# Kernel tuning notes

Hardware: AMD Instinct MI355X
Metric: run time of the kernel (lower is better)

## Reference

```python
import jax, jax.numpy as jnp
import numpy as np

B, S, D = 2, 2048, 1024
H = 16
DH = D // H  # 64


def setup_inputs() -> dict:
    key = jax.random.key(0)
    ks = jax.random.split(key, 5)
    scale = 0.02
    x = jax.random.normal(ks[0], (B, S, D), dtype=jnp.float32)
    W_qkv = jax.random.normal(ks[1], (D, 3 * D), dtype=jnp.float32) * scale
    b_qkv = jnp.zeros((3 * D,), dtype=jnp.float32)
    W_out = jax.random.normal(ks[2], (D, D), dtype=jnp.float32) * scale
    b_out = jnp.zeros((D,), dtype=jnp.float32)
    return {"x": x, "W_qkv": W_qkv, "b_qkv": b_qkv, "W_out": W_out, "b_out": b_out}


def reference(x, W_qkv, b_qkv, W_out, b_out):
    # Fused QKV projection: [B,S,D] @ [D,3D] -> [B,S,3D]
    qkv = jnp.einsum('bsd,df->bsf', x, W_qkv) + b_qkv
    q, k, v = qkv[:, :, :D], qkv[:, :, D:2 * D], qkv[:, :, 2 * D:]
    # Split heads: [B,S,D] -> [B,H,S,DH]
    def split(t):
        return t.reshape(B, S, H, DH).transpose(0, 2, 1, 3)
    q, k, v = split(q), split(k), split(v)
    # Scaled dot-product attention (naive, full score matrix as in source)
    scores = jnp.einsum('bhqd,bhkd->bhqk', q, k) / jnp.sqrt(jnp.float32(DH))
    probs = jax.nn.softmax(scores, axis=-1)  # mask=None, dropout eval-mode identity
    attn = jnp.einsum('bhqk,bhkd->bhqd', probs, v)
    # Merge heads: [B,H,S,DH] -> [B,S,D]
    attn = attn.transpose(0, 2, 1, 3).reshape(B, S, D)
    out = jnp.einsum('bsd,de->bse', attn, W_out) + b_out
    return out
```

## Files before the change

### kernel.cpp

```cpp
#include <hip/hip_runtime.h>

typedef _Float16 half8  __attribute__((ext_vector_type(8)));
typedef _Float16 half4  __attribute__((ext_vector_type(4)));
typedef float    floatx4  __attribute__((ext_vector_type(4)));
typedef float    floatx16 __attribute__((ext_vector_type(16)));
typedef unsigned int uint4v __attribute__((ext_vector_type(4)));

constexpr int B_ = 2, S_ = 2048, D_ = 1024, H_ = 16, M_ = 4096;
constexpr int NR_ = B_ * H_ * S_;
constexpr float QSCALE = 0.18033688011112042f;
constexpr int KVB = 64;
constexpr int HT = 16;

__device__ __forceinline__ void gload16(const void* g, void* l) {
  __builtin_amdgcn_global_load_lds((const __attribute__((address_space(1))) void*)g,
                                   (__attribute__((address_space(3))) void*)l, 16, 0, 0);
}

__global__ __launch_bounds__(256) void cast_f32_f16(const float* __restrict__ in,
                                                    _Float16* __restrict__ out, int n8) {
  int i = blockIdx.x * 256 + threadIdx.x;
  if (i >= n8) return;
  float4 a = reinterpret_cast<const float4*>(in)[2 * i];
  float4 b = reinterpret_cast<const float4*>(in)[2 * i + 1];
  half8 h;
  h[0] = (_Float16)a.x; h[1] = (_Float16)a.y; h[2] = (_Float16)a.z; h[3] = (_Float16)a.w;
  h[4] = (_Float16)b.x; h[5] = (_Float16)b.y; h[6] = (_Float16)b.z; h[7] = (_Float16)b.w;
  reinterpret_cast<half8*>(out)[i] = h;
}

__global__ __launch_bounds__(256) void transpose_cast2(const float* __restrict__ W0,
                                                       _Float16* __restrict__ WT0,
                                                       const float* __restrict__ W1,
                                                       _Float16* __restrict__ WT1) {
  __shared__ float Ws[64][65];
  const int z = blockIdx.z;
  const int NW = z ? D_ : 3 * D_;
  if (blockIdx.x * 64 >= NW) return;
  const float* W = z ? W1 : W0;
  _Float16* WT = z ? WT1 : WT0;
  const int K = D_, N = NW;
  const int n0 = blockIdx.x * 64, k0 = blockIdx.y * 64;
  const int t = threadIdx.x;
#pragma unroll
  for (int i = 0; i < 4; i++) {
    int idx = t + 256 * i;
    int r = idx >> 4, c4 = idx & 15;
    float4 v = *reinterpret_cast<const float4*>(W + (size_t)(k0 + r) * N + n0 + c4 * 4);
    Ws[r][c4 * 4 + 0] = v.x; Ws[r][c4 * 4 + 1] = v.y;
    Ws[r][c4 * 4 + 2] = v.z; Ws[r][c4 * 4 + 3] = v.w;
  }
  __syncthreads();
#pragma unroll
  for (int i = 0; i < 2; i++) {
    int idx = t + 256 * i;
    int r = idx >> 3, ck = idx & 7;
    half8 h;
#pragma unroll
    for (int j = 0; j < 8; j++) h[j] = (_Float16)Ws[ck * 8 + j][r];
    *reinterpret_cast<half8*>(WT + (size_t)(n0 + r) * K + k0 + ck * 8) = h;
  }
}

__global__ __launch_bounds__(512, 2) void gemm256_mfma(
    const _Float16* __restrict__ A, const _Float16* __restrict__ BT,
    const float* __restrict__ bias, _Float16* __restrict__ Cout,
    int M, int N, int K, float scale_lo, int ncut) {
  extern __shared__ char smem[];
  const int tid = threadIdx.x, w = tid >> 6, lane = tid & 63;
  const int wm = w >> 2, wn = w & 3;

  const int nwg = gridDim.x, cpx = nwg >> 3;
  const int wg = (blockIdx.x & 7) * cpx + (blockIdx.x >> 3);
  const int nbx = N / 192;
  const int bx = wg % nbx, by = wg / nbx;
  const int m0 = by * 256, n0 = bx * 192;

  const int NT = K >> 6;

  auto stageA1 = [&](int buf, int kt, int i) {
    const int k0 = kt * 64;
    char* Ad = smem + buf * 32768;
    int idx = tid + 512 * i;
    int r = idx >> 3, c = idx & 7, cs = c ^ (r & 7);
    gload16(A + (size_t)(m0 + r) * K + k0 + cs * 8, Ad + idx * 16);
  };
  auto stageB1 = [&](int buf, int kt, int i) {
    const int k0 = kt * 64;
    char* Bd = smem + 65536 + buf * 24576;
    int idx = tid + 512 * i;
    int r = idx >> 3, c = idx & 7, cs = c ^ (r & 7);
    gload16(BT + (size_t)(n0 + r) * K + k0 + cs * 8, Bd + idx * 16);
  };

  floatx4 acc[8][3] = {};

#pragma unroll
  for (int i = 0; i < 4; i++) stageA1(0, 0, i);
#pragma unroll
  for (int i = 0; i < 3; i++) stageB1(0, 0, i);

  for (int kt = 0; kt < NT; ++kt) {
    const int p = kt & 1;
    asm volatile("s_waitcnt vmcnt(0)" ::: "memory");
    __builtin_amdgcn_s_barrier();
    __builtin_amdgcn_sched_barrier(0);

    const char* Ab = smem + p * 32768;
    const char* Bb = smem + 65536 + p * 24576;
    const bool more = (kt + 1 < NT);
#pragma unroll
    for (int q = 0; q < 4; q++) {
      half8 af[2][2], bf[3][2];
#pragma unroll
      for (int e = 0; e < 2; e++)
#pragma unroll
        for (int ks = 0; ks < 2; ks++) {
          int row = wm * 128 + (2 * q + e) * 16 + (lane & 15);
          int ch = (ks * 4 + (lane >> 4)) ^ (row & 7);
          af[e][ks] = *reinterpret_cast<const half8*>(Ab + row * 128 + ch * 16);
        }
#pragma unroll
      for (int n = 0; n < 3; n++)
#pragma unroll
        for (int ks = 0; ks < 2; ks++) {
          int row = wn * 48 + n * 16 + (lane & 15);
          int ch = (ks * 4 + (lane >> 4)) ^ (row & 7);
          bf[n][ks] = *reinterpret_cast<const half8*>(Bb + row * 128 + ch * 16);
        }
      if (more) {
        if (q == 0)      { stageA1(p ^ 1, kt + 1, 0); stageA1(p ^ 1, kt + 1, 1); }
        else if (q == 1) { stageA1(p ^ 1, kt + 1, 2); stageA1(p ^ 1, kt + 1, 3); }
        else if (q == 2) { stageB1(p ^ 1, kt + 1, 0); stageB1(p ^ 1, kt + 1, 1); }
        else             { stageB1(p ^ 1, kt + 1, 2); }
      }
      __builtin_amdgcn_s_setprio(1);
#pragma unroll
      for (int ks = 0; ks < 2; ks++)
#pragma unroll
        for (int e = 0; e < 2; e++)
#pragma unroll
          for (int n = 0; n < 3; n++)
            acc[2 * q + e][n] = __builtin_amdgcn_mfma_f32_16x16x32_f16(
                af[e][ks], bf[n][ks], acc[2 * q + e][n], 0, 0, 0);
      __builtin_amdgcn_s_setprio(0);
    }
    __builtin_amdgcn_sched_barrier(0);
    __builtin_amdgcn_s_barrier();
  }

#pragma unroll
  for (int mf = 0; mf < 8; mf++)
#pragma unroll
    for (int n = 0; n < 3; n++) {
      int col = n0 + wn * 48 + n * 16 + (lane & 15);
      float bv = bias[col];
      float sc = (col < ncut) ? scale_lo : 1.0f;
#pragma unroll
      for (int reg = 0; reg < 4; reg++) {
        int row = m0 + wm * 128 + mf * 16 + (lane >> 4) * 4 + reg;
        Cout[(size_t)row * N + col] = (_Float16)((acc[mf][n][reg] + bv) * sc);
      }
    }
}

template <bool OUT_HALF>
__global__ __launch_bounds__(256) void gemm_mfma(const _Float16* __restrict__ A,
                                                 const _Float16* __restrict__ BT,
                                                 const float* __restrict__ bias,
                                                 void* __restrict__ Cout,
                                                 int M, int N, int K,
                                                 float scale_lo, int ncut) {
  __shared__ _Float16 As[128 * 64];
  __shared__ _Float16 Bs[128 * 64];
  const int t = threadIdx.x, w = t >> 6, lane = t & 63;
  const int m0 = blockIdx.y * 128, n0 = blockIdx.x * 128;
  const int wr = (w >> 1) * 64, wc = (w & 1) * 64;

  floatx4 acc[4][4] = {};

  for (int k0 = 0; k0 < K; k0 += 64) {
    __syncthreads();
#pragma unroll
    for (int i = 0; i < 4; i++) {
      int idx = t + 256 * i;
      int r = idx >> 3, c = idx & 7;
      int cs = c ^ (r & 7);
      gload16(A + (size_t)(m0 + r) * K + k0 + cs * 8, (char*)As + idx * 16);
      gload16(BT + (size_t)(n0 + r) * K + k0 + cs * 8, (char*)Bs + idx * 16);
    }
    __syncthreads();
#pragma unroll
    for (int ks = 0; ks < 2; ks++) {
      half8 af[4], bf[4];
#pragma unroll
      for (int r = 0; r < 4; r++) {
        int row = wr + r * 16 + (lane & 15);
        int ch = (ks * 4 + (lane >> 4)) ^ (row & 7);
        af[r] = *reinterpret_cast<const half8*>((const char*)As + row * 128 + ch * 16);
      }
#pragma unroll
      for (int c = 0; c < 4; c++) {
        int row = wc + c * 16 + (lane & 15);
        int ch = (ks * 4 + (lane >> 4)) ^ (row & 7);
        bf[c] = *reinterpret_cast<const half8*>((const char*)Bs + row * 128 + ch * 16);
      }
#pragma unroll
      for (int r = 0; r < 4; r++)
#pragma unroll
        for (int c = 0; c < 4; c++)
          acc[r][c] = __builtin_amdgcn_mfma_f32_16x16x32_f16(af[r], bf[c], acc[r][c], 0, 0, 0);
    }
  }

#pragma unroll
  for (int r = 0; r < 4; r++)
#pragma unroll
    for (int c = 0; c < 4; c++) {
      int col = n0 + wc + c * 16 + (lane & 15);
      float bv = bias[col];
      float sc = (col < ncut) ? scale_lo : 1.0f;
#pragma unroll
      for (int reg = 0; reg < 4; reg++) {
        int row = m0 + wr + r * 16 + (lane >> 4) * 4 + reg;
        float v = (acc[r][c][reg] + bv) * sc;
        if (OUT_HALF)
          reinterpret_cast<_Float16*>(Cout)[(size_t)row * N + col] = (_Float16)v;
        else
          reinterpret_cast<float*>(Cout)[(size_t)row * N + col] = v;
      }
    }
}

__global__ __launch_bounds__(256) void v_transpose(const _Float16* __restrict__ qkv,
                                                   _Float16* __restrict__ Vt) {
  __shared__ _Float16 Vs[64][72];
  const int s0 = blockIdx.x * 64, bh = blockIdx.y;
  const int b = bh >> 4, h = bh & 15;
  const int t = threadIdx.x;
#pragma unroll
  for (int i = 0; i < 2; i++) {
    int idx = t + 256 * i;
    int r = idx >> 3, c = idx & 7;
    half8 v = *reinterpret_cast<const half8*>(
        qkv + (size_t)(b * S_ + s0 + r) * (3 * D_) + 2 * D_ + h * 64 + c * 8);
    *reinterpret_cast<half8*>(&Vs[r][c * 8]) = v;
  }
  __syncthreads();
#pragma unroll
  for (int i = 0; i < 2; i++) {
    int idx = t + 256 * i;
    int d = idx >> 3, c = idx & 7;
    half8 o;
#pragma unroll
    for (int j = 0; j < 8; j++) o[j] = Vs[c * 8 + j][d];
    *reinterpret_cast<half8*>(Vt + ((size_t)bh * 64 + d) * S_ + s0 + c * 8) = o;
  }
}

__global__ __launch_bounds__(256, 4) void flash_mfma(const _Float16* __restrict__ qkv,
                                                     const _Float16* __restrict__ Vt,
                                                     _Float16* __restrict__ Opart,
                                                     float* __restrict__ keys) {
  const int qt = blockIdx.x, h = blockIdx.y;
  const int b = blockIdx.z >> 1, sp = blockIdx.z & 1;
  const int t = threadIdx.x, w = t >> 6, lane = t & 63;
  const int lo = lane & 31, hi = lane >> 5;

  __shared__ _Float16 Ks[2][KVB * 64];
  __shared__ _Float16 Vts[2][64 * KVB];

  const int qrow = qt * 128 + w * 32 + lo;
  const _Float16* qbase = qkv + (size_t)(b * S_ + qrow) * (3 * D_) + h * 64;
  half8 qf[4];
#pragma unroll
  for (int kd = 0; kd < 4; kd++)
    qf[kd] = *reinterpret_cast<const half8*>(qbase + kd * 16 + hi * 8);
  asm volatile("" : "+v"(qf[0]), "+v"(qf[1]), "+v"(qf[2]), "+v"(qf[3]));

  const size_t kbase = (size_t)(b * S_) * (3 * D_) + D_ + h * 64;
  const size_t vbase = (size_t)(b * H_ + h) * 64 * S_;
  const int kvbase = sp * (S_ / 2);

  auto stage = [&](int buf, int tile) {
    const int kv0 = kvbase + tile * KVB;
    const _Float16* kg = qkv + kbase + (size_t)kv0 * (3 * D_);
#pragma unroll
    for (int p = 0; p < 2; p++) {
      int idx = t + 256 * p;
      int r = idx >> 3, c = idx & 7, cs = c ^ (r & 7);
      gload16(kg + (size_t)r * (3 * D_) + cs * 8, (char*)&Ks[buf][0] + idx * 16);
    }
    const _Float16* vg = Vt + vbase + kv0;
#pragma unroll
    for (int p = 0; p < 2; p++) {
      int idx = t + 256 * p;
      int r = idx >> 3, c = idx & 7, cs = c ^ (r & 7);
      gload16(vg + (size_t)r * S_ + cs * 8, (char*)&Vts[buf][0] + idx * 16);
    }
  };

  floatx16 o0, o1;
#pragma unroll
  for (int r = 0; r < 16; r++) { o0[r] = 0.f; o1[r] = 0.f; }
  float m = -1e30f, l = 0.f;

  stage(0, 0);

  for (int tt = 0; tt < HT; ++tt) {
    const int cb = tt & 1;
    stage(cb ^ 1, (tt + 1) & (HT - 1));
    asm volatile("s_waitcnt vmcnt(4)" ::: "memory");
    __builtin_amdgcn_s_barrier();
    __builtin_amdgcn_sched_barrier(0);

    const char* kb2 = (const char*)&Ks[cb][0];
    floatx16 s0v, s1v;
#pragma unroll
    for (int r = 0; r < 16; r++) { s0v[r] = 0.f; s1v[r] = 0.f; }
    __builtin_amdgcn_s_setprio(1);
#pragma unroll
    for (int kd = 0; kd < 4; kd++) {
      int r0 = lo, r1 = 32 + lo;
      half8 k0f = *reinterpret_cast<const half8*>(
          kb2 + r0 * 128 + (((kd * 2 + hi) ^ (r0 & 7)) * 16));
      half8 k1f = *reinterpret_cast<const half8*>(
          kb2 + r1 * 128 + (((kd * 2 + hi) ^ (r1 & 7)) * 16));
      s0v = __builtin_amdgcn_mfma_f32_32x32x16_f16(k0f, qf[kd], s0v, 0, 0, 0);
      s1v = __builtin_amdgcn_mfma_f32_32x32x16_f16(k1f, qf[kd], s1v, 0, 0, 0);
    }
    __builtin_amdgcn_s_setprio(0);

    float pm = -1e30f;
#pragma unroll
    for (int r = 0; r < 16; r++) pm = fmaxf(pm, fmaxf(s0v[r], s1v[r]));
    pm = fmaxf(pm, __shfl_xor(pm, 32));
    if (!__all(pm <= m + 8.0f)) {
      float mn = fmaxf(m, pm);
      float al = __builtin_amdgcn_exp2f(m - mn);
      m = mn; l *= al;
#pragma unroll
      for (int r = 0; r < 16; r++) { o0[r] *= al; o1[r] *= al; }
    }
    float rs = 0.f;
#pragma unroll
    for (int r = 0; r < 16; r++) {
      s0v[r] = __builtin_amdgcn_exp2f(s0v[r] - m);
      s1v[r] = __builtin_amdgcn_exp2f(s1v[r] - m);
      rs += s0v[r] + s1v[r];
    }
    rs += __shfl_xor(rs, 32);
    l += rs;

    half8 pf0a, pf0b, pf1a, pf1b;
    {
      unsigned a0 = __builtin_bit_cast(unsigned, __builtin_amdgcn_cvt_pkrtz(s0v[0], s0v[1]));
      unsigned b0 = __builtin_bit_cast(unsigned, __builtin_amdgcn_cvt_pkrtz(s0v[4], s0v[5]));
      unsigned a1 = __builtin_bit_cast(unsigned, __builtin_amdgcn_cvt_pkrtz(s0v[2], s0v[3]));
      unsigned b1 = __builtin_bit_cast(unsigned, __builtin_amdgcn_cvt_pkrtz(s0v[6], s0v[7]));
      asm("v_permlane32_swap_b32 %0, %1" : "+v"(a0), "+v"(b0));
      asm("v_permlane32_swap_b32 %0, %1" : "+v"(a1), "+v"(b1));
      uint4v u; u[0] = a0; u[1] = a1; u[2] = b0; u[3] = b1;
      pf0a = __builtin_bit_cast(half8, u);
      a0 = __builtin_bit_cast(unsigned, __builtin_amdgcn_cvt_pkrtz(s0v[8], s0v[9]));
      b0 = __builtin_bit_cast(unsigned, __builtin_amdgcn_cvt_pkrtz(s0v[12], s0v[13]));
      a1 = __builtin_bit_cast(unsigned, __builtin_amdgcn_cvt_pkrtz(s0v[10], s0v[11]));
      b1 = __builtin_bit_cast(unsigned, __builtin_amdgcn_cvt_pkrtz(s0v[14], s0v[15]));
      asm("v_permlane32_swap_b32 %0, %1" : "+v"(a0), "+v"(b0));
      asm("v_permlane32_swap_b32 %0, %1" : "+v"(a1), "+v"(b1));
      u[0] = a0; u[1] = a1; u[2] = b0; u[3] = b1;
      pf0b = __builtin_bit_cast(half8, u);
      a0 = __builtin_bit_cast(unsigned, __builtin_amdgcn_cvt_pkrtz(s1v[0], s1v[1]));
      b0 = __builtin_bit_cast(unsigned, __builtin_amdgcn_cvt_pkrtz(s1v[4], s1v[5]));
      a1 = __builtin_bit_cast(unsigned, __builtin_amdgcn_cvt_pkrtz(s1v[2], s1v[3]));
      b1 = __builtin_bit_cast(unsigned, __builtin_amdgcn_cvt_pkrtz(s1v[6], s1v[7]));
      asm("v_permlane32_swap_b32 %0, %1" : "+v"(a0), "+v"(b0));
      asm("v_permlane32_swap_b32 %0, %1" : "+v"(a1), "+v"(b1));
      u[0] = a0; u[1] = a1; u[2] = b0; u[3] = b1;
      pf1a = __builtin_bit_cast(half8, u);
      a0 = __builtin_bit_cast(unsigned, __builtin_amdgcn_cvt_pkrtz(s1v[8], s1v[9]));
      b0 = __builtin_bit_cast(unsigned, __builtin_amdgcn_cvt_pkrtz(s1v[12], s1v[13]));
      a1 = __builtin_bit_cast(unsigned, __builtin_amdgcn_cvt_pkrtz(s1v[10], s1v[11]));
      b1 = __builtin_bit_cast(unsigned, __builtin_amdgcn_cvt_pkrtz(s1v[14], s1v[15]));
      asm("v_permlane32_swap_b32 %0, %1" : "+v"(a0), "+v"(b0));
      asm("v_permlane32_swap_b32 %0, %1" : "+v"(a1), "+v"(b1));
      u[0] = a0; u[1] = a1; u[2] = b0; u[3] = b1;
      pf1b = __builtin_bit_cast(half8, u);
    }

    const char* vb2 = (const char*)&Vts[cb][0];
    __builtin_amdgcn_s_setprio(1);
#pragma unroll
    for (int ks = 0; ks < 4; ks++) {
      half8 pf = (ks == 0) ? pf0a : (ks == 1) ? pf0b : (ks == 2) ? pf1a : pf1b;
      const int ch = ks * 2 + hi;
      half8 vf0 = *reinterpret_cast<const half8*>(vb2 + lo * 128 + ((ch ^ (lo & 7)) * 16));
      half8 vf1 = *reinterpret_cast<const half8*>(vb2 + (lo + 32) * 128 + ((ch ^ (lo & 7)) * 16));
      o0 = __builtin_amdgcn_mfma_f32_32x32x16_f16(vf0, pf, o0, 0, 0, 0);
      o1 = __builtin_amdgcn_mfma_f32_32x32x16_f16(vf1, pf, o1, 0, 0, 0);
    }
    __builtin_amdgcn_s_setprio(0);

    __builtin_amdgcn_sched_barrier(0);
    __builtin_amdgcn_s_barrier();
  }

  float inv = 1.0f / l;
  const int gr = (b * H_ + h) * S_ + qrow;
  _Float16* ob = Opart + ((size_t)sp * NR_ + gr) * 64;
#pragma unroll
  for (int mt = 0; mt < 2; mt++)
#pragma unroll
    for (int rq = 0; rq < 4; rq++) {
      half4 v;
#pragma unroll
      for (int e = 0; e < 4; e++) v[e] = (_Float16)(((mt ? o1 : o0)[4 * rq + e]) * inv);
      *reinterpret_cast<half4*>(ob + 32 * mt + 8 * rq + 4 * hi) = v;
    }
  if (hi == 0) keys[sp * NR_ + gr] = m + __log2f(l);
}

__global__ __launch_bounds__(256) void flash_combine(const _Float16* __restrict__ Opart,
                                                     const float* __restrict__ keys,
                                                     _Float16* __restrict__ attn_out) {
  const int gr = blockIdx.x * 256 + threadIdx.x;
  const float k0 = keys[gr], k1 = keys[NR_ + gr];
  const float mx = fmaxf(k0, k1);
  const float w0 = __builtin_amdgcn_exp2f(k0 - mx);
  const float w1 = __builtin_amdgcn_exp2f(k1 - mx);
  const float inv = 1.0f / (w0 + w1);
  const float a0 = w0 * inv, a1 = w1 * inv;
  const int bh = gr >> 11, qs = gr & 2047, b = bh >> 4, h = bh & 15;
  const half8* p0 = reinterpret_cast<const half8*>(Opart + (size_t)gr * 64);
  const half8* p1 = reinterpret_cast<const half8*>(Opart + ((size_t)NR_ + gr) * 64);
  half8* ob = reinterpret_cast<half8*>(
      attn_out + ((size_t)(b * S_ + qs)) * D_ + h * 64);
#pragma unroll
  for (int j = 0; j < 8; j++) {
    half8 x0 = p0[j], x1 = p1[j];
    half8 o;
#pragma unroll
    for (int e = 0; e < 8; e++)
      o[e] = (_Float16)(a0 * (float)x0[e] + a1 * (float)x1[e]);
    ob[j] = o;
  }
}

extern "C" void kernel_launch(void* const* d_in, const int* in_sizes, int n_in,
                              void* d_out, int out_size, void* d_ws, size_t ws_size,
                              hipStream_t stream) {
  const float* x     = (const float*)d_in[0];
  const float* W_qkv = (const float*)d_in[1];
  const float* b_qkv = (const float*)d_in[2];
  const float* W_out = (const float*)d_in[3];
  const float* b_out = (const float*)d_in[4];
  float* out = (float*)d_out;

  _Float16* xh    = (_Float16*)d_ws;
  _Float16* qkvh  = xh + (size_t)M_ * D_;
  _Float16* Vth   = qkvh + (size_t)M_ * 3 * D_;
  _Float16* WoT   = Vth + (size_t)B_ * H_ * 64 * S_;
  _Float16* WqT   = WoT + (size_t)D_ * D_;
  _Float16* Opart = WqT;
  float*    keys  = (float*)(Opart + (size_t)2 * NR_ * 64);
  _Float16* atth  = xh;

  cast_f32_f16<<<(M_ * D_ / 8 + 255) / 256, 256, 0, stream>>>(x, xh, M_ * D_ / 8);
  transpose_cast2<<<dim3(3 * D_ / 64, D_ / 64, 2), 256, 0, stream>>>(
      W_qkv, WqT, W_out, WoT);

  gemm256_mfma<<<256, 512, 114688, stream>>>(
      xh, WqT, b_qkv, qkvh, M_, 3 * D_, D_, QSCALE, D_);

  v_transpose<<<dim3(S_ / 64, B_ * H_), 256, 0, stream>>>(qkvh, Vth);

  flash_mfma<<<dim3(S_ / 128, H_, B_ * 2), 256, 0, stream>>>(qkvh, Vth, Opart, keys);

  flash_combine<<<NR_ / 256, 256, 0, stream>>>(Opart, keys, atth);

  gemm_mfma<false><<<dim3(D_ / 128, M_ / 128), 256, 0, stream>>>(
      atth, WoT, b_out, out, M_, D_, D_, 1.0f, 0);
}
```

Measured before the change: 135.1 us.

## Load V fragments directly from global into registers instead of staging in LDS

Drops the double-buffered V tile in shared memory. Each wave now reads its V fragments from global memory straight into registers, prefetching one k-slice ahead inside the PV MFMA loop. The row max and row sum become tree reductions instead of serial chains, and the occupancy hint drops from 4 to 3 blocks per CU to free registers. This removes LDS traffic and LDS space for V, but every wave now fetches the same V tile separately, so global and L2 traffic rises. Global latency is also exposed right next to the MFMAs.

```diff
diff --git a/kernel.cpp b/kernel.cpp
--- a/kernel.cpp
+++ b/kernel.cpp
@@ -258,7 +258,7 @@
   }
 }
 
-__global__ __launch_bounds__(256, 4) void flash_mfma(const _Float16* __restrict__ qkv,
+__global__ __launch_bounds__(256, 3) void flash_mfma(const _Float16* __restrict__ qkv,
                                                      const _Float16* __restrict__ Vt,
                                                      _Float16* __restrict__ Opart,
                                                      float* __restrict__ keys) {
@@ -268,7 +268,6 @@
   const int lo = lane & 31, hi = lane >> 5;
 
   __shared__ _Float16 Ks[2][KVB * 64];
-  __shared__ _Float16 Vts[2][64 * KVB];
 
   const int qrow = qt * 128 + w * 32 + lo;
   const _Float16* qbase = qkv + (size_t)(b * S_ + qrow) * (3 * D_) + h * 64;
@@ -282,7 +281,7 @@
   const size_t vbase = (size_t)(b * H_ + h) * 64 * S_;
   const int kvbase = sp * (S_ / 2);
 
-  auto stage = [&](int buf, int tile) {
+  auto stageK = [&](int buf, int tile) {
     const int kv0 = kvbase + tile * KVB;
     const _Float16* kg = qkv + kbase + (size_t)kv0 * (3 * D_);
 #pragma unroll
@@ -291,13 +290,6 @@
       int r = idx >> 3, c = idx & 7, cs = c ^ (r & 7);
       gload16(kg + (size_t)r * (3 * D_) + cs * 8, (char*)&Ks[buf][0] + idx * 16);
     }
-    const _Float16* vg = Vt + vbase + kv0;
-#pragma unroll
-    for (int p = 0; p < 2; p++) {
-      int idx = t + 256 * p;
-      int r = idx >> 3, c = idx & 7, cs = c ^ (r & 7);
-      gload16(vg + (size_t)r * S_ + cs * 8, (char*)&Vts[buf][0] + idx * 16);
-    }
   };
 
   floatx16 o0, o1;
@@ -305,11 +297,17 @@
   for (int r = 0; r < 16; r++) { o0[r] = 0.f; o1[r] = 0.f; }
   float m = -1e30f, l = 0.f;
 
-  stage(0, 0);
+  stageK(0, 0);
 
   for (int tt = 0; tt < HT; ++tt) {
     const int cb = tt & 1;
-    stage(cb ^ 1, (tt + 1) & (HT - 1));
+    const int kv0 = kvbase + tt * KVB;
+    const _Float16* vgl = Vt + vbase + kv0;
+
+    half8 va = *reinterpret_cast<const half8*>(vgl + (size_t)lo * S_ + hi * 8);
+    half8 vb = *reinterpret_cast<const half8*>(vgl + (size_t)(lo + 32) * S_ + hi * 8);
+
+    stageK(cb ^ 1, (tt + 1) & (HT - 1));
     asm volatile("s_waitcnt vmcnt(4)" ::: "memory");
     __builtin_amdgcn_s_barrier();
     __builtin_amdgcn_sched_barrier(0);
@@ -331,9 +329,17 @@
     }
     __builtin_amdgcn_s_setprio(0);
 
-    float pm = -1e30f;
-#pragma unroll
-    for (int r = 0; r < 16; r++) pm = fmaxf(pm, fmaxf(s0v[r], s1v[r]));
+    float tm[16];
+#pragma unroll
+    for (int r = 0; r < 16; r++) tm[r] = fmaxf(s0v[r], s1v[r]);
+    float u0 = fmaxf(fmaxf(tm[0], tm[1]), tm[2]);
+    float u1 = fmaxf(fmaxf(tm[3], tm[4]), tm[5]);
+    float u2 = fmaxf(fmaxf(tm[6], tm[7]), tm[8]);
+    float u3 = fmaxf(fmaxf(tm[9], tm[10]), tm[11]);
+    float u4 = fmaxf(fmaxf(tm[12], tm[13]), tm[14]);
+    float pm = fmaxf(fmaxf(u0, u1), u2);
+    pm = fmaxf(fmaxf(pm, u3), u4);
+    pm = fmaxf(pm, tm[15]);
     pm = fmaxf(pm, __shfl_xor(pm, 32));
     if (!__all(pm <= m + 8.0f)) {
       float mn = fmaxf(m, pm);
@@ -342,13 +348,18 @@
 #pragma unroll
       for (int r = 0; r < 16; r++) { o0[r] *= al; o1[r] *= al; }
     }
-    float rs = 0.f;
+    float rr[16];
 #pragma unroll
     for (int r = 0; r < 16; r++) {
       s0v[r] = __builtin_amdgcn_exp2f(s0v[r] - m);
       s1v[r] = __builtin_amdgcn_exp2f(s1v[r] - m);
-      rs += s0v[r] + s1v[r];
-    }
+      rr[r] = s0v[r] + s1v[r];
+    }
+#pragma unroll
+    for (int st = 8; st >= 1; st >>= 1)
+#pragma unroll
+      for (int r = 0; r < st; r++) rr[r] += rr[r + st];
+    float rs = rr[0];
     rs += __shfl_xor(rs, 32);
     l += rs;
 
@@ -388,16 +399,19 @@
       pf1b = __builtin_bit_cast(half8, u);
     }
 
-    const char* vb2 = (const char*)&Vts[cb][0];
     __builtin_amdgcn_s_setprio(1);
 #pragma unroll
     for (int ks = 0; ks < 4; ks++) {
       half8 pf = (ks == 0) ? pf0a : (ks == 1) ? pf0b : (ks == 2) ? pf1a : pf1b;
-      const int ch = ks * 2 + hi;
-      half8 vf0 = *reinterpret_cast<const half8*>(vb2 + lo * 128 + ((ch ^ (lo & 7)) * 16));
-      half8 vf1 = *reinterpret_cast<const half8*>(vb2 + (lo + 32) * 128 + ((ch ^ (lo & 7)) * 16));
-      o0 = __builtin_amdgcn_mfma_f32_32x32x16_f16(vf0, pf, o0, 0, 0, 0);
-      o1 = __builtin_amdgcn_mfma_f32_32x32x16_f16(vf1, pf, o1, 0, 0, 0);
+      half8 vna, vnb;
+      if (ks < 3) {
+        int off = (ks + 1) * 16 + hi * 8;
+        vna = *reinterpret_cast<const half8*>(vgl + (size_t)lo * S_ + off);
+        vnb = *reinterpret_cast<const half8*>(vgl + (size_t)(lo + 32) * S_ + off);
+      }
+      o0 = __builtin_amdgcn_mfma_f32_32x32x16_f16(va, pf, o0, 0, 0, 0);
+      o1 = __builtin_amdgcn_mfma_f32_32x32x16_f16(vb, pf, o1, 0, 0, 0);
+      if (ks < 3) { va = vna; vb = vnb; }
     }
     __builtin_amdgcn_s_setprio(0);
 
```

Measured after the change: 168.6 us. +24.8%, slower.

## Double-buffer output-projection GEMM and tree-reduce softmax max and sum

Applied to the files above, without the earlier changes.

The output-projection GEMM now uses double-buffered LDS, issuing the next K-tile's global-to-LDS loads between MFMA groups so loads overlap compute. It also remaps workgroup IDs in groups of eight, which appears aimed at XCD/L2 locality, and drops the unused half-output and scale template paths. Separately, the flash kernel's row max and row sum reductions become shallow trees instead of serial chains, shortening dependency latency. The cost is more LDS (64KB) and register pressure, which could limit occupancy.

```diff
diff --git a/kernel.cpp b/kernel.cpp
--- a/kernel.cpp
+++ b/kernel.cpp
@@ -164,70 +164,102 @@
     }
 }
 
-template <bool OUT_HALF>
-__global__ __launch_bounds__(256) void gemm_mfma(const _Float16* __restrict__ A,
-                                                 const _Float16* __restrict__ BT,
-                                                 const float* __restrict__ bias,
-                                                 void* __restrict__ Cout,
-                                                 int M, int N, int K,
-                                                 float scale_lo, int ncut) {
-  __shared__ _Float16 As[128 * 64];
-  __shared__ _Float16 Bs[128 * 64];
-  const int t = threadIdx.x, w = t >> 6, lane = t & 63;
-  const int m0 = blockIdx.y * 128, n0 = blockIdx.x * 128;
-  const int wr = (w >> 1) * 64, wc = (w & 1) * 64;
+__global__ __launch_bounds__(256, 2) void gemm128_mfma(
+    const _Float16* __restrict__ A, const _Float16* __restrict__ BT,
+    const float* __restrict__ bias, float* __restrict__ Cout,
+    int M, int N, int K) {
+  extern __shared__ char smem[];
+  const int tid = threadIdx.x, w = tid >> 6, lane = tid & 63;
+  const int wm = w >> 1, wn = w & 1;
+
+  const int nwg = gridDim.x, cpx = nwg >> 3;
+  const int wg = (blockIdx.x & 7) * cpx + (blockIdx.x >> 3);
+  const int nbx = N >> 7;
+  const int bx = wg % nbx, by = wg / nbx;
+  const int m0 = by * 128, n0 = bx * 128;
+
+  const int NT = K >> 6;
+
+  auto stageA1 = [&](int buf, int kt, int i) {
+    const int k0 = kt * 64;
+    char* Ad = smem + buf * 16384;
+    int idx = tid + 256 * i;
+    int r = idx >> 3, c = idx & 7, cs = c ^ (r & 7);
+    gload16(A + (size_t)(m0 + r) * K + k0 + cs * 8, Ad + idx * 16);
+  };
+  auto stageB1 = [&](int buf, int kt, int i) {
+    const int k0 = kt * 64;
+    char* Bd = smem + 32768 + buf * 16384;
+    int idx = tid + 256 * i;
+    int r = idx >> 3, c = idx & 7, cs = c ^ (r & 7);
+    gload16(BT + (size_t)(n0 + r) * K + k0 + cs * 8, Bd + idx * 16);
+  };
 
   floatx4 acc[4][4] = {};
 
-  for (int k0 = 0; k0 < K; k0 += 64) {
-    __syncthreads();
-#pragma unroll
-    for (int i = 0; i < 4; i++) {
-      int idx = t + 256 * i;
-      int r = idx >> 3, c = idx & 7;
-      int cs = c ^ (r & 7);
-      gload16(A + (size_t)(m0 + r) * K + k0 + cs * 8, (char*)As + idx * 16);
-      gload16(BT + (size_t)(n0 + r) * K + k0 + cs * 8, (char*)Bs + idx * 16);
-    }
-    __syncthreads();
-#pragma unroll
-    for (int ks = 0; ks < 2; ks++) {
-      half8 af[4], bf[4];
-#pragma unroll
-      for (int r = 0; r < 4; r++) {
-        int row = wr + r * 16 + (lane & 15);
+#pragma unroll
+  for (int i = 0; i < 4; i++) stageA1(0, 0, i);
+#pragma unroll
+  for (int i = 0; i < 4; i++) stageB1(0, 0, i);
+
+  for (int kt = 0; kt < NT; ++kt) {
+    const int p = kt & 1;
+    asm volatile("s_waitcnt vmcnt(0)" ::: "memory");
+    __builtin_amdgcn_s_barrier();
+    __builtin_amdgcn_sched_barrier(0);
+
+    const char* Ab = smem + p * 16384;
+    const char* Bb = smem + 32768 + p * 16384;
+    const bool more = (kt + 1 < NT);
+
+    half8 bf[4][2];
+#pragma unroll
+    for (int n = 0; n < 4; n++)
+#pragma unroll
+      for (int ks = 0; ks < 2; ks++) {
+        int row = wn * 64 + n * 16 + (lane & 15);
         int ch = (ks * 4 + (lane >> 4)) ^ (row & 7);
-        af[r] = *reinterpret_cast<const half8*>((const char*)As + row * 128 + ch * 16);
+        bf[n][ks] = *reinterpret_cast<const half8*>(Bb + row * 128 + ch * 16);
       }
-#pragma unroll
-      for (int c = 0; c < 4; c++) {
-        int row = wc + c * 16 + (lane & 15);
+
+#pragma unroll
+    for (int q = 0; q < 4; q++) {
+      half8 af[2];
+#pragma unroll
+      for (int ks = 0; ks < 2; ks++) {
+        int row = wm * 64 + q * 16 + (lane & 15);
         int ch = (ks * 4 + (lane >> 4)) ^ (row & 7);
-        bf[c] = *reinterpret_cast<const half8*>((const char*)Bs + row * 128 + ch * 16);
+        af[ks] = *reinterpret_cast<const half8*>(Ab + row * 128 + ch * 16);
       }
-#pragma unroll
-      for (int r = 0; r < 4; r++)
-#pragma unroll
-        for (int c = 0; c < 4; c++)
-          acc[r][c] = __builtin_amdgcn_mfma_f32_16x16x32_f16(af[r], bf[c], acc[r][c], 0, 0, 0);
-    }
-  }
-
-#pragma unroll
-  for (int r = 0; r < 4; r++)
-#pragma unroll
-    for (int c = 0; c < 4; c++) {
-      int col = n0 + wc + c * 16 + (lane & 15);
+      if (more) {
+        if (q == 0)      { stageA1(p ^ 1, kt + 1, 0); stageA1(p ^ 1, kt + 1, 1); }
+        else if (q == 1) { stageA1(p ^ 1, kt + 1, 2); stageA1(p ^ 1, kt + 1, 3); }
+        else if (q == 2) { stageB1(p ^ 1, kt + 1, 0); stageB1(p ^ 1, kt + 1, 1); }
+        else             { stageB1(p ^ 1, kt + 1, 2); stageB1(p ^ 1, kt + 1, 3); }
+      }
+      __builtin_amdgcn_s_setprio(1);
+#pragma unroll
+      for (int ks = 0; ks < 2; ks++)
+#pragma unroll
+        for (int n = 0; n < 4; n++)
+          acc[q][n] = __builtin_amdgcn_mfma_f32_16x16x32_f16(
+              af[ks], bf[n][ks], acc[q][n], 0, 0, 0);
+      __builtin_amdgcn_s_setprio(0);
+    }
+    __builtin_amdgcn_sched_barrier(0);
+    __builtin_amdgcn_s_barrier();
+  }
+
+#pragma unroll
+  for (int q = 0; q < 4; q++)
+#pragma unroll
+    for (int n = 0; n < 4; n++) {
+      int col = n0 + wn * 64 + n * 16 + (lane & 15);
       float bv = bias[col];
-      float sc = (col < ncut) ? scale_lo : 1.0f;
 #pragma unroll
       for (int reg = 0; reg < 4; reg++) {
-        int row = m0 + wr + r * 16 + (lane >> 4) * 4 + reg;
-        float v = (acc[r][c][reg] + bv) * sc;
-        if (OUT_HALF)
-          reinterpret_cast<_Float16*>(Cout)[(size_t)row * N + col] = (_Float16)v;
-        else
-          reinterpret_cast<float*>(Cout)[(size_t)row * N + col] = v;
+        int row = m0 + wm * 64 + q * 16 + (lane >> 4) * 4 + reg;
+        Cout[(size_t)row * N + col] = acc[q][n][reg] + bv;
       }
     }
 }
@@ -331,9 +363,17 @@
     }
     __builtin_amdgcn_s_setprio(0);
 
-    float pm = -1e30f;
-#pragma unroll
-    for (int r = 0; r < 16; r++) pm = fmaxf(pm, fmaxf(s0v[r], s1v[r]));
+    float tm[16];
+#pragma unroll
+    for (int r = 0; r < 16; r++) tm[r] = fmaxf(s0v[r], s1v[r]);
+    float u0 = fmaxf(fmaxf(tm[0], tm[1]), tm[2]);
+    float u1 = fmaxf(fmaxf(tm[3], tm[4]), tm[5]);
+    float u2 = fmaxf(fmaxf(tm[6], tm[7]), tm[8]);
+    float u3 = fmaxf(fmaxf(tm[9], tm[10]), tm[11]);
+    float u4 = fmaxf(fmaxf(tm[12], tm[13]), tm[14]);
+    float pm = fmaxf(fmaxf(u0, u1), u2);
+    pm = fmaxf(fmaxf(pm, u3), u4);
+    pm = fmaxf(pm, tm[15]);
     pm = fmaxf(pm, __shfl_xor(pm, 32));
     if (!__all(pm <= m + 8.0f)) {
       float mn = fmaxf(m, pm);
@@ -342,13 +382,18 @@
 #pragma unroll
       for (int r = 0; r < 16; r++) { o0[r] *= al; o1[r] *= al; }
     }
-    float rs = 0.f;
+    float rr[16];
 #pragma unroll
     for (int r = 0; r < 16; r++) {
       s0v[r] = __builtin_amdgcn_exp2f(s0v[r] - m);
       s1v[r] = __builtin_amdgcn_exp2f(s1v[r] - m);
-      rs += s0v[r] + s1v[r];
-    }
+      rr[r] = s0v[r] + s1v[r];
+    }
+#pragma unroll
+    for (int st = 8; st >= 1; st >>= 1)
+#pragma unroll
+      for (int r = 0; r < st; r++) rr[r] += rr[r + st];
+    float rs = rr[0];
     rs += __shfl_xor(rs, 32);
     l += rs;
 
@@ -478,6 +523,6 @@
 
   flash_combine<<<NR_ / 256, 256, 0, stream>>>(Opart, keys, atth);
 
-  gemm_mfma<false><<<dim3(D_ / 128, M_ / 128), 256, 0, stream>>>(
-      atth, WoT, b_out, out, M_, D_, D_, 1.0f, 0);
-}
+  gemm128_mfma<<<256, 256, 65536, stream>>>(
+      atth, WoT, b_out, out, M_, D_, D_);
+}
```

New measurement: 128.4 us. 5.0% less time.
